# Optimization experiments

Hardware: AMD Instinct MI355X
Metric: run time of the kernel (lower is better)

## Reference

```python
import jax, jax.numpy as jnp
import numpy as np

B, L, W, S, STEPS, VOCAB, NLAB = 1024, 128, 512, 8, 12, 32, 10

def setup_inputs() -> dict:
    key = jax.random.key(0)
    ks = jax.random.split(key, 24)
    def nrm(k, shape, scale=0.05):
        return jax.random.normal(k, shape, jnp.float32) * scale
    x = jax.random.randint(ks[0], (B, L), 0, VOCAB)
    embed = nrm(ks[1], (VOCAB, W), 0.1).at[0].set(0.0)  # padding_idx=0
    return {
        'x': x,
        'embed': embed,
        'W_mix': nrm(ks[2], (W, 3 * W)), 'b_mix': jnp.zeros((W,), jnp.float32),
        'W_in': nrm(ks[3], (S, W, 2 * W)), 'b_in': jnp.zeros((S, W), jnp.float32),
        'W_link': nrm(ks[4], (S, W, W)), 'b_link': jnp.zeros((S, W), jnp.float32),
        'W_ih': nrm(ks[5], (S, 3 * W, W)), 'b_ih': jnp.zeros((S, 3 * W), jnp.float32),
        'W_hh': nrm(ks[6], (S, 3 * W, W)), 'b_hh': jnp.zeros((S, 3 * W), jnp.float32),
        'W_gate': nrm(ks[7], (S, 1, W)), 'b_gate': jnp.zeros((S, 1), jnp.float32),
        'phase': nrm(ks[8], (S, W), 0.5), 'prism_gain': jnp.zeros((S, W), jnp.float32),
        'W_delta': nrm(ks[9], (S, W, W)), 'b_delta': jnp.zeros((S, W), jnp.float32),
        'decay_param': jnp.zeros((), jnp.float32),
        'W_out': nrm(ks[10], (NLAB, W)), 'b_out': jnp.zeros((NLAB,), jnp.float32),
    }

def _encode(x, embed, W_mix, b_mix):
    emb = embed[x]                                          # [B,L,W]
    mask = (x != 0).astype(jnp.float32)[..., None]          # [B,L,1]
    summed = (emb * mask).sum(1)
    denom = jnp.maximum(mask.sum(1), 1.0)
    mean = summed / denom
    maxed = jnp.where(mask == 0, -10000.0, emb).max(1)
    maxed = jnp.where(jnp.isfinite(maxed), maxed, 0.0)
    last_idx = jnp.maximum(mask[..., 0].sum(1).astype(jnp.int32) - 1, 0)
    last = jnp.take_along_axis(emb, last_idx[:, None, None], axis=1)[:, 0]
    cat = jnp.concatenate([mean, maxed, last], -1)          # [B,3W]
    return jnp.tanh(cat @ W_mix.T + b_mix)

def _forward(x, embed, W_mix, b_mix, W_in, b_in, W_link, b_link, W_ih, b_ih,
             W_hh, b_hh, W_gate, b_gate, phase, prism_gain, W_delta, b_delta,
             decay_param, W_out, b_out):
    summary = _encode(x, embed, W_mix, b_mix)               # [B,W]
    decay = jax.nn.sigmoid(decay_param)
    inv_sqrt_s = np.float32(1.0 / np.sqrt(S))
    gain = jax.nn.softplus(prism_gain)[None]                # [1,S,W]

    def step(carry, _):
        h, hs = carry
        shared = jnp.concatenate([h, summary], -1)          # conditioned: [B,2W]
        f0 = jnp.tanh(jnp.einsum('swi,bi->bsw', W_in, shared) + b_in)      # [B,S,W]
        prev = jnp.roll(f0, 1, axis=1)                      # sparse ring: feats[(i-1)%S]
        feats = jnp.tanh(f0 + jnp.einsum('sow,bsw->bso', W_link, prev) + b_link)
        # recurrent side pockets: per-side GRUCell (torch gate order r,z,n)
        gi = jnp.einsum('sgw,bsw->bsg', W_ih, feats) + b_ih
        gh = jnp.einsum('sgw,bsw->bsg', W_hh, hs) + b_hh
        ir, iz, inn = jnp.split(gi, 3, -1)
        hr, hz, hn = jnp.split(gh, 3, -1)
        r = jax.nn.sigmoid(ir + hr)
        z = jax.nn.sigmoid(iz + hz)
        n = jnp.tanh(inn + r * hn)
        hs_new = (1.0 - z) * n + z * hs                     # [B,S,W]
        feat = hs_new
        gate = jax.nn.sigmoid(jnp.einsum('sow,bsw->bso', W_gate, feat) + b_gate)  # [B,S,1]
        feat = jnp.cos(feat + phase[None]) ** 2 * gain      # prismion
        upd = gate * jnp.tanh(jnp.einsum('sow,bsw->bso', W_delta, feat) + b_delta)
        delta = upd.sum(1) * inv_sqrt_s
        h_new = jnp.tanh(h * decay + delta)
        return (h_new, hs_new), None

    hs0 = jnp.zeros((B, S, W), jnp.float32)
    (h, _), _ = jax.lax.scan(step, (summary, hs0), None, length=STEPS)
    return h @ W_out.T + b_out                               # [B,10]

def reference(x, embed, W_mix, b_mix, W_in, b_in, W_link, b_link, W_ih, b_ih,
              W_hh, b_hh, W_gate, b_gate, phase, prism_gain, W_delta, b_delta,
              decay_param, W_out, b_out):
    return _forward(x, embed, W_mix, b_mix, W_in, b_in, W_link, b_link, W_ih,
                    b_ih, W_hh, b_hh, W_gate, b_gate, phase, prism_gain,
                    W_delta, b_delta, decay_param, W_out, b_out)
```

## Files before the change

kernel.cpp:

```cpp
#include <hip/hip_runtime.h>
#include <hip/hip_bf16.h>


typedef unsigned short u16;
typedef __attribute__((ext_vector_type(8))) short short8;
typedef __attribute__((ext_vector_type(4))) float f32x4;

__device__ __forceinline__ float bf2f(u16 v) {
    union { unsigned int u; float f; } x; x.u = ((unsigned int)v) << 16; return x.f;
}
__device__ __forceinline__ u16 f2bf(float f) {
    union { float f; unsigned int u; } x; x.f = f;
    unsigned int u = x.u;
    return (u16)((u + 0x7FFFu + ((u >> 16) & 1u)) >> 16);
}
__device__ __forceinline__ float fsig(float v) {
    return __builtin_amdgcn_rcpf(1.f + __expf(-v));
}
__device__ __forceinline__ float ftanh(float v) {
    return 1.f - 2.f * __builtin_amdgcn_rcpf(__expf(2.f * v) + 1.f);
}
__device__ __forceinline__ float fsoftplus(float v) {
    return (v > 20.f) ? v : __logf(1.f + __expf(v));
}

union U4 { ushort4 v; u16 e[4]; };

__device__ __forceinline__ void gload_lds16(const u16* g, u16* l) {
    __builtin_amdgcn_global_load_lds(
        (const __attribute__((address_space(1))) unsigned int*)g,
        (__attribute__((address_space(3))) unsigned int*)l, 16, 0, 0);
}

__device__ __forceinline__ int sane16(u16 u) {
    if ((u & 0x7FFF) == 0) return 1;
    int e = (u >> 7) & 0xFF;
    return (e >= 0x33 && e <= 0x43) ? 1 : 0;
}
__global__ __launch_bounds__(256) void detect_k(const u16* __restrict__ raw,
                                                int* __restrict__ flag) {
    const int t = threadIdx.x;
    int c = sane16(raw[1024 + t * 2]) + sane16(raw[1024 + t * 2 + 1]);
#pragma unroll
    for (int off = 32; off; off >>= 1) c += __shfl_down(c, off, 64);
    __shared__ int red[4];
    if ((t & 63) == 0) red[t >> 6] = c;
    __syncthreads();
    if (t == 0) *flag = (red[0] + red[1] + red[2] + red[3] >= 448) ? 1 : 0;
}

struct CT { const void* src[20]; int n[20]; int off[20]; };
__global__ __launch_bounds__(256) void conv_k(CT ct, u16* __restrict__ dstBase,
                                              const int* __restrict__ flag) {
    const int isbf = *flag;
    const int gid = blockIdx.x * 256 + threadIdx.x;
    const int stride = gridDim.x * 256;
    for (int tn = 0; tn < 20; ++tn) {
        const int n = ct.n[tn];
        const int n4 = n >> 2;
        u16* dst = dstBase + ct.off[tn];
        if (!isbf) {
            const float* s = (const float*)ct.src[tn];
            for (int i = gid; i < n4; i += stride) {
                f32x4 v = *(const f32x4*)(s + i * 4);
                *(ushort4*)(dst + i * 4) =
                    make_ushort4(f2bf(v[0]), f2bf(v[1]), f2bf(v[2]), f2bf(v[3]));
            }
            if (gid < (n & 3)) { int i = n4 * 4 + gid; dst[i] = f2bf(s[i]); }
        } else {
            const u16* s = (const u16*)ct.src[tn];
            for (int i = gid; i < n4; i += stride)
                *(ushort4*)(dst + i * 4) = *(const ushort4*)(s + i * 4);
            if (gid < (n & 3)) { int i = n4 * 4 + gid; dst[i] = s[i]; }
        }
    }
}

__global__ __launch_bounds__(256) void pack_k(const u16* __restrict__ Wih,
                                              const u16* __restrict__ Whh,
                                              u16* __restrict__ Wcat) {
    long i = ((long)blockIdx.x * 256 + threadIdx.x) * 8;
    if (i >= 8L * 1536 * 512) return;
    long sg = i >> 9;
    long k  = i & 511;
    *(short8*)(Wcat + sg * 1024 + k)       = *(const short8*)(Wih + i);
    *(short8*)(Wcat + sg * 1024 + 512 + k) = *(const short8*)(Whh + i);
}

struct GP {
    const u16* A;  long lda; long aOff[8];
    const u16* Bw; long ldb; long bwOff[8];
    const u16* bias; long biasOff[8];
    const u16* add; long ldadd; long addOff;
    const float* gate_pre;
    const u16* bgate;
    void* C; long ldc; long cOff[8];
    float* C2;
    u16* C3;
    int K; int nt;
};

template<int EPI, int MT>
__global__ __launch_bounds__(256) void gemm_k(GP p) {
    constexpr int MW   = MT / 32;
    constexpr int AITS = MT / 32;
    __shared__ __align__(16) u16 lA[2][MT * 64];
    __shared__ __align__(16) u16 lB[2][128 * 64];
    const int t    = threadIdx.x;
    const int lane = t & 63;
    const int wv   = t >> 6;
    const int bx   = blockIdx.x;
    const int z    = bx / p.nt;
    const int n0   = (bx - z * p.nt) * 128;
    const int m0   = blockIdx.y * MT;

    const u16* Ab = p.A + p.aOff[z] + (long)m0 * p.lda;
    const u16* Bb = p.Bw + p.bwOff[z] + (long)n0 * p.ldb;

    f32x4 acc[MW][4];
#pragma unroll
    for (int i = 0; i < MW; i++)
#pragma unroll
        for (int j = 0; j < 4; j++) acc[i][j] = (f32x4){0.f, 0.f, 0.f, 0.f};

    const int wm   = (wv & 1) * (MT / 2);
    const int wn   = (wv >> 1) * 64;
    const int fr   = lane & 15;
    const int quad = lane >> 4;

    const int nk = p.K >> 6;
#pragma unroll
    for (int it = 0; it < AITS; ++it) {
        int flat = it * 256 + t, row = flat >> 3, src = (flat & 7) ^ (row & 7);
        gload_lds16(Ab + (long)row * p.lda + src * 8, &lA[0][flat * 8]);
    }
#pragma unroll
    for (int it = 0; it < 4; ++it) {
        int flat = it * 256 + t, row = flat >> 3, src = (flat & 7) ^ (row & 7);
        gload_lds16(Bb + (long)row * p.ldb + src * 8, &lB[0][flat * 8]);
    }
    __syncthreads();

    for (int kt = 0; kt < nk; ++kt) {
        const int cur = kt & 1, nxt = cur ^ 1;
        if (kt + 1 < nk) {
            const long kb = (long)(kt + 1) * 64;
#pragma unroll
            for (int it = 0; it < AITS; ++it) {
                int flat = it * 256 + t, row = flat >> 3, src = (flat & 7) ^ (row & 7);
                gload_lds16(Ab + (long)row * p.lda + kb + src * 8, &lA[nxt][flat * 8]);
            }
#pragma unroll
            for (int it = 0; it < 4; ++it) {
                int flat = it * 256 + t, row = flat >> 3, src = (flat & 7) ^ (row & 7);
                gload_lds16(Bb + (long)row * p.ldb + kb + src * 8, &lB[nxt][flat * 8]);
            }
        }
#pragma unroll
        for (int kk = 0; kk < 2; ++kk) {
            const int q = kk * 4 + quad;
            short8 aF[MW], bF[4];
#pragma unroll
            for (int mi = 0; mi < MW; mi++) {
                int row = wm + mi * 16 + fr;
                aF[mi] = *(const short8*)&lA[cur][row * 64 + (q ^ (row & 7)) * 8];
            }
#pragma unroll
            for (int ni = 0; ni < 4; ni++) {
                int row = wn + ni * 16 + fr;
                bF[ni] = *(const short8*)&lB[cur][row * 64 + (q ^ (row & 7)) * 8];
            }
#pragma unroll
            for (int mi = 0; mi < MW; mi++)
#pragma unroll
                for (int ni = 0; ni < 4; ni++)
                    acc[mi][ni] = __builtin_amdgcn_mfma_f32_16x16x32_bf16(
                        aF[mi], bF[ni], acc[mi][ni], 0, 0, 0);
        }
        __syncthreads();
    }

    float sgv[MW][4];
    if (EPI == 3) {
#pragma unroll
        for (int mi = 0; mi < MW; mi++)
#pragma unroll
            for (int r = 0; r < 4; r++) {
                long row = m0 + wm + mi * 16 + quad * 4 + r;
                sgv[mi][r] = fsig(p.gate_pre[row * 8 + z] + bf2f(p.bgate[z]));
            }
    }

#pragma unroll
    for (int mi = 0; mi < MW; mi++) {
#pragma unroll
        for (int ni = 0; ni < 4; ni++) {
            const int mg = m0 + wm + mi * 16 + quad * 4;
            const int ng = n0 + wn + ni * 16 + fr;
#pragma unroll
            for (int r = 0; r < 4; r++) {
                float v = acc[mi][ni][r];
                const long row = mg + r;
                if (EPI == 1) {
                    float ad = bf2f(p.add[z * p.addOff + row * p.ldadd + ng]);
                    v = ftanh(v + ad + bf2f(p.bias[p.biasOff[z] + ng]));
                    ((u16*)p.C)[p.cOff[z] + row * p.ldc + ng] = f2bf(v);
                } else if (EPI == 3) {
                    v = ftanh(v + bf2f(p.bias[p.biasOff[z] + ng])) * sgv[mi][r];
                    ((u16*)p.C)[p.cOff[z] + row * p.ldc + ng] = f2bf(v);
                } else if (EPI == 4) {
                    v = ftanh(v + bf2f(p.bias[ng]));
                    u16 b = f2bf(v);
                    ((u16*)p.C)[row * 512 + ng] = b;
                    p.C3[row * 512 + ng] = b;
                    p.C2[row * 512 + ng] = v;
                } else if (EPI == 6) {
                    v = v + bf2f(p.bias[p.biasOff[z] + ng]);
                    ((u16*)p.C)[p.cOff[z] + row * p.ldc + ng] = f2bf(v);
                } else {
                    float ad = bf2f(p.add[row * p.ldadd + ng]);
                    v = ftanh(v + ad);
                    ((u16*)p.C)[row * p.ldc + ng] = f2bf(v);
                }
            }
        }
    }
}

struct GGP {
    const u16* fhs_in;
    u16* fhs_out;
    const u16* Wcat;
    const u16* b_ih;
    const u16* b_hh;
    u16* prism;
    float* gate_pre;
    const u16* Wg;
    const u16* phase;
    const u16* pgain;
};

__global__ __launch_bounds__(256, 4) void grug_k(GGP p) {
    __shared__ __align__(16) u16 sA[2][64 * 32];
    __shared__ __align__(16) u16 sW[2][3][64 * 32];
    const int t    = threadIdx.x;
    const int lane = t & 63;
    const int wv   = t >> 6;
    const int s    = blockIdx.x >> 3;
    const int w0   = (blockIdx.x & 7) * 64;
    const int m0   = blockIdx.y * 64;
    const int fr   = lane & 15;
    const int quad = lane >> 4;
    const int wn   = wv * 16;

    const u16* Ab = p.fhs_in + (long)m0 * 8192 + s * 1024;
    const u16* Wb = p.Wcat + (long)s * 1536 * 1024;

    f32x4 acc[4][4];
#pragma unroll
    for (int q = 0; q < 4; q++)
#pragma unroll
        for (int mi = 0; mi < 4; mi++) acc[q][mi] = (f32x4){0.f,0.f,0.f,0.f};

    const int arow = t >> 2, ac4 = t & 3, asrc = ac4 ^ ((arow >> 1) & 3);

    auto stageA = [&](int buf, long kb) {
        gload_lds16(Ab + (long)arow * 8192 + kb + asrc * 8, &sA[buf][t * 8]);
    };
    auto stageW = [&](int buf, long kb) {
#pragma unroll
        for (int q = 0; q < 3; q++) {
            long g = (long)(q * 512 + w0 + arow);
            gload_lds16(Wb + g * 1024 + kb + asrc * 8, &sW[buf][q][t * 8]);
        }
    };

    stageA(0, 0); stageW(0, 0);
    __syncthreads();

    for (int kt = 0; kt < 32; ++kt) {
        const int cur = kt & 1, nxt = cur ^ 1;
        if (kt + 1 < 32) { stageA(nxt, (long)(kt + 1) * 32); stageW(nxt, (long)(kt + 1) * 32); }
        const int qsel = (kt < 16) ? 2 : 3;
        short8 aF[4], bF[3];
#pragma unroll
        for (int mi = 0; mi < 4; mi++) {
            int row = mi * 16 + fr;
            aF[mi] = *(const short8*)&sA[cur][row * 32 + ((quad ^ ((row >> 1) & 3)) & 3) * 8];
        }
#pragma unroll
        for (int q = 0; q < 3; q++) {
            int row = wn + fr;
            bF[q] = *(const short8*)&sW[cur][q][row * 32 + ((quad ^ ((row >> 1) & 3)) & 3) * 8];
        }
#pragma unroll
        for (int mi = 0; mi < 4; mi++) {
            acc[0][mi] = __builtin_amdgcn_mfma_f32_16x16x32_bf16(aF[mi], bF[0], acc[0][mi], 0, 0, 0);
            acc[1][mi] = __builtin_amdgcn_mfma_f32_16x16x32_bf16(aF[mi], bF[1], acc[1][mi], 0, 0, 0);
            if (qsel == 2)
                acc[2][mi] = __builtin_amdgcn_mfma_f32_16x16x32_bf16(aF[mi], bF[2], acc[2][mi], 0, 0, 0);
            else
                acc[3][mi] = __builtin_amdgcn_mfma_f32_16x16x32_bf16(aF[mi], bF[2], acc[3][mi], 0, 0, 0);
        }
        __syncthreads();
    }

    const u16* bih = p.b_ih + (long)s * 1536;
    const u16* bhh = p.b_hh + (long)s * 1536;
    float gp[4][4];
#pragma unroll
    for (int mi = 0; mi < 4; mi++)
#pragma unroll
        for (int r = 0; r < 4; r++) gp[mi][r] = 0.f;

    {
        const int col = w0 + wn + fr;
        const float br  = bf2f(bih[col])        + bf2f(bhh[col]);
        const float bz  = bf2f(bih[512 + col])  + bf2f(bhh[512 + col]);
        const float bin = bf2f(bih[1024 + col]);
        const float bhn = bf2f(bhh[1024 + col]);
        const float ph  = bf2f(p.phase[s * 512 + col]);
        const float gain = fsoftplus(bf2f(p.pgain[s * 512 + col]));
        const float wg  = bf2f(p.Wg[s * 512 + col]);
#pragma unroll
        for (int mi = 0; mi < 4; mi++) {
#pragma unroll
            for (int r = 0; r < 4; r++) {
                const long b = m0 + mi * 16 + quad * 4 + r;
                float rv = fsig(acc[0][mi][r] + br);
                float zv = fsig(acc[1][mi][r] + bz);
                float nv = ftanh(acc[2][mi][r] + bin + rv * (acc[3][mi][r] + bhn));
                float hold = bf2f(p.fhs_in[b * 8192 + s * 1024 + 512 + col]);
                float hv = (1.f - zv) * nv + zv * hold;
                p.fhs_out[b * 8192 + s * 1024 + 512 + col] = f2bf(hv);
                float c = __cosf(hv + ph);
                p.prism[b * 4096 + s * 512 + col] = f2bf(c * c * gain);
                gp[mi][r] += wg * hv;
            }
        }
    }
#pragma unroll
    for (int m = 1; m < 16; m <<= 1)
#pragma unroll
        for (int mi = 0; mi < 4; mi++)
#pragma unroll
            for (int r = 0; r < 4; r++) gp[mi][r] += __shfl_xor(gp[mi][r], m, 64);
    if (fr == 0) {
#pragma unroll
        for (int mi = 0; mi < 4; mi++)
#pragma unroll
            for (int r = 0; r < 4; r++) {
                long b = m0 + mi * 16 + quad * 4 + r;
                atomicAdd(&p.gate_pre[b * 8 + s], gp[mi][r]);
            }
    }
}

__global__ __launch_bounds__(256) void encode_k(const int* __restrict__ x,
                                                const u16* __restrict__ embed,
                                                u16* __restrict__ cat) {
    __shared__ int toks[128];
    __shared__ int cnt_s;
    const int b = blockIdx.x, t = threadIdx.x;
    if (t < 128) toks[t] = x[b * 128 + t];
    __syncthreads();
    if (t == 0) {
        int c = 0;
        for (int l = 0; l < 128; l++) c += (toks[l] != 0);
        cnt_s = c;
    }
    __syncthreads();
    const int cnt = cnt_s;
    const int lastTok = toks[cnt > 0 ? cnt - 1 : 0];
    for (int w = t; w < 512; w += 256) {
        float sum = 0.f, mx = -10000.f;
        for (int l = 0; l < 128; l++) {
            int tok = toks[l];
            if (tok != 0) {
                float e = bf2f(embed[tok * 512 + w]);
                sum += e;
                mx = fmaxf(mx, e);
            }
        }
        float mean = sum / (float)(cnt > 0 ? cnt : 1);
        float last = bf2f(embed[lastTok * 512 + w]);
        cat[(long)b * 1536 + w]        = f2bf(mean);
        cat[(long)b * 1536 + 512 + w]  = f2bf(mx);
        cat[(long)b * 1536 + 1024 + w] = f2bf(last);
    }
}

__global__ __launch_bounds__(256) void hupd_k(const u16* __restrict__ upd,
                                              float* __restrict__ h,
                                              u16* __restrict__ h_b,
                                              const u16* __restrict__ decay_p) {
    const int idx = blockIdx.x * 256 + threadIdx.x;
    const int b = idx >> 9, w = idx & 511;
    const long base = (long)b * 4096 + w;
    float dsum = 0.f;
#pragma unroll
    for (int s = 0; s < 8; s++) dsum += bf2f(upd[base + s * 512]);
    const float decay = fsig(bf2f(decay_p[0]));
    const float hv = ftanh(h[idx] * decay + dsum * 0.35355339059327373f);
    h[idx] = hv;
    h_b[idx] = f2bf(hv);
}

__global__ __launch_bounds__(64) void out_k(const float* __restrict__ h,
                                            const u16* __restrict__ Wout,
                                            const u16* __restrict__ bout,
                                            void* __restrict__ out,
                                            const int* __restrict__ flag) {
    const int b = blockIdx.x, lane = threadIdx.x;
    const int isbf = *flag;
    for (int j = 0; j < 10; j++) {
        float p = 0.f;
#pragma unroll
        for (int k = 0; k < 8; k++) {
            int w = lane + k * 64;
            p += h[(long)b * 512 + w] * bf2f(Wout[j * 512 + w]);
        }
#pragma unroll
        for (int off = 32; off; off >>= 1) p += __shfl_down(p, off, 64);
        if (lane == 0) {
            float val = p + bf2f(bout[j]);
            if (isbf) ((u16*)out)[b * 10 + j] = f2bf(val);
            else      ((float*)out)[b * 10 + j] = val;
        }
    }
}

extern "C" void kernel_launch(void* const* d_in, const int* in_sizes, int n_in,
                              void* d_out, int out_size, void* d_ws, size_t ws_size,
                              hipStream_t stream) {
    (void)n_in; (void)out_size; (void)ws_size;
    const int* x = (const int*)d_in[0];

    char* pp = (char*)d_ws;
    auto carve = [&](size_t n) { char* r = pp; pp += (n + 255) & ~(size_t)255; return (void*)r; };

    CT ct;
    size_t ctot = 0;
    for (int i = 0; i < 20; i++) {
        ct.src[i] = d_in[i + 1];
        ct.n[i]   = in_sizes[i + 1];
        ct.off[i] = (int)ctot;
        ctot += ((size_t)in_sizes[i + 1] + 15) & ~(size_t)15;
    }
    u16* canon = (u16*)carve(ctot * 2);
    const u16* embed  = canon + ct.off[0];
    const u16* W_mix  = canon + ct.off[1];
    const u16* b_mix  = canon + ct.off[2];
    const u16* W_in   = canon + ct.off[3];
    const u16* b_in   = canon + ct.off[4];
    const u16* W_link = canon + ct.off[5];
    const u16* b_link = canon + ct.off[6];
    const u16* W_ih   = canon + ct.off[7];
    const u16* b_ih   = canon + ct.off[8];
    const u16* W_hh   = canon + ct.off[9];
    const u16* b_hh   = canon + ct.off[10];
    const u16* W_gate = canon + ct.off[11];
    const u16* b_gate = canon + ct.off[12];
    const u16* phase  = canon + ct.off[13];
    const u16* pgain  = canon + ct.off[14];
    const u16* W_delta= canon + ct.off[15];
    const u16* b_delta= canon + ct.off[16];
    const u16* decayp = canon + ct.off[17];
    const u16* W_out  = canon + ct.off[18];
    const u16* b_out  = canon + ct.off[19];

    int*   flag   = (int*)  carve(256);
    u16*   Wcat   = (u16*)  carve((size_t)8 * 1536 * 1024 * 2);
    u16*   cat    = (u16*)  carve((size_t)1024 * 1536 * 2);
    u16*   h_b    = (u16*)  carve((size_t)1024 * 512 * 2);
    u16*   summ_b = (u16*)  carve((size_t)1024 * 512 * 2);
    float* h      = (float*)carve((size_t)1024 * 512 * 4);
    u16*   cin    = (u16*)  carve((size_t)1024 * 4096 * 2);
    u16*   f0     = (u16*)  carve((size_t)1024 * 4096 * 2);
    u16*   fhs0   = (u16*)  carve((size_t)1024 * 8192 * 2);
    u16*   fhs1   = (u16*)  carve((size_t)1024 * 8192 * 2);
    u16*   prism  = (u16*)  carve((size_t)1024 * 4096 * 2);
    u16*   upd    = (u16*)  carve((size_t)1024 * 4096 * 2);
    float* gate_pre = (float*)carve((size_t)1024 * 8 * 4);

    (void)hipMemsetAsync(fhs0, 0, (size_t)1024 * 8192 * 2, stream);
    (void)hipMemsetAsync(fhs1, 0, (size_t)1024 * 8192 * 2, stream);

    detect_k<<<dim3(1), dim3(256), 0, stream>>>((const u16*)d_in[1], flag);
    conv_k<<<dim3(1024), dim3(256), 0, stream>>>(ct, canon, flag);
    pack_k<<<dim3(3072), dim3(256), 0, stream>>>(W_ih, W_hh, Wcat);
    encode_k<<<dim3(1024), dim3(256), 0, stream>>>(x, embed, cat);

    {
        GP p{}; p.A = cat; p.lda = 1536; p.Bw = W_mix; p.ldb = 1536;
        p.bias = b_mix; p.C = h_b; p.ldc = 512; p.C2 = h; p.C3 = summ_b;
        p.K = 1536; p.nt = 4;
        gemm_k<4, 64><<<dim3(4, 16, 1), dim3(256), 0, stream>>>(p);
    }
    {
        GP p{}; p.A = summ_b; p.lda = 512; p.Bw = W_in + 512; p.ldb = 1024;
        p.bias = b_in; p.C = cin; p.ldc = 4096; p.K = 512; p.nt = 32;
        gemm_k<6, 64><<<dim3(32, 16, 1), dim3(256), 0, stream>>>(p);
    }

    for (int step = 0; step < 12; ++step) {
        u16* fhs_cur = (step & 1) ? fhs1 : fhs0;
        u16* fhs_nxt = (step & 1) ? fhs0 : fhs1;
        {
            GP p{}; p.A = h_b; p.lda = 512; p.Bw = W_in; p.ldb = 1024;
            p.add = cin; p.ldadd = 4096; p.C = f0; p.ldc = 4096;
            p.K = 512; p.nt = 32;
            gemm_k<7, 64><<<dim3(32, 16, 1), dim3(256), 0, stream>>>(p);
        }
        {
            GP p{}; p.A = f0; p.lda = 4096;
            for (int s = 0; s < 8; s++) p.aOff[s] = (long)((s + 7) & 7) * 512;
            p.Bw = W_link; p.ldb = 512;
            for (int s = 0; s < 8; s++) p.bwOff[s] = (long)s * 512 * 512;
            p.bias = b_link;
            for (int s = 0; s < 8; s++) p.biasOff[s] = (long)s * 512;
            p.add = f0; p.ldadd = 4096; p.addOff = 512;
            p.C = fhs_cur; p.ldc = 8192;
            for (int s = 0; s < 8; s++) p.cOff[s] = (long)s * 1024;
            p.K = 512; p.nt = 4;
            gemm_k<1, 64><<<dim3(32, 16, 1), dim3(256), 0, stream>>>(p);
        }
        (void)hipMemsetAsync(gate_pre, 0, (size_t)1024 * 8 * 4, stream);
        {
            GGP g{};
            g.fhs_in = fhs_cur; g.fhs_out = fhs_nxt; g.Wcat = Wcat;
            g.b_ih = b_ih; g.b_hh = b_hh; g.prism = prism; g.gate_pre = gate_pre;
            g.Wg = W_gate; g.phase = phase; g.pgain = pgain;
            grug_k<<<dim3(64, 16, 1), dim3(256), 0, stream>>>(g);
        }
        {
            GP p{}; p.A = prism; p.lda = 4096;
            for (int s = 0; s < 8; s++) p.aOff[s] = (long)s * 512;
            p.Bw = W_delta; p.ldb = 512;
            for (int s = 0; s < 8; s++) p.bwOff[s] = (long)s * 512 * 512;
            p.bias = b_delta;
            for (int s = 0; s < 8; s++) p.biasOff[s] = (long)s * 512;
            p.gate_pre = gate_pre; p.bgate = b_gate;
            p.C = upd; p.ldc = 4096;
            for (int s = 0; s < 8; s++) p.cOff[s] = (long)s * 512;
            p.K = 512; p.nt = 4;
            gemm_k<3, 64><<<dim3(32, 16, 1), dim3(256), 0, stream>>>(p);
        }
        hupd_k<<<dim3(2048), dim3(256), 0, stream>>>(upd, h, h_b, decayp);
    }

    out_k<<<dim3(1024), dim3(64), 0, stream>>>(h, W_out, b_out, d_out, flag);
}
```

Before: 1.715 ms.

## Swizzle GEMM blocks across XCDs, widen GRU tile, fold gate_pre reset into hupd

Adds an optional workgroup-id swizzle to the batched GEMM so consecutive workgroups map to different stacks and n-tiles. This is meant to improve L2 reuse of weight tiles on the multi-XCD part. The GRU kernel now runs 512 threads and covers 128 output columns per block, sharing one activation tile across twice as many weight rows. Its block order is also remapped so the stack index varies fastest. The per-step memset of gate_pre is replaced by zeroing inside hupd_k, which removes one launch per step. The 512-thread launch with a minimum of 4 blocks per CU tightens the register budget and may cause spills.

```diff
diff --git a/kernel.cpp b/kernel.cpp
--- a/kernel.cpp
+++ b/kernel.cpp
@@ -100,7 +100,7 @@
     int K; int nt;
 };
 
-template<int EPI, int MT>
+template<int EPI, int MT, int SWZ>
 __global__ __launch_bounds__(256) void gemm_k(GP p) {
     constexpr int MW   = MT / 32;
     constexpr int AITS = MT / 32;
@@ -109,10 +109,15 @@
     const int t    = threadIdx.x;
     const int lane = t & 63;
     const int wv   = t >> 6;
-    const int bx   = blockIdx.x;
+    int bx = blockIdx.x, byy = blockIdx.y;
+    if (SWZ) {
+        int wgid = bx + (byy << 5);
+        bx  = ((wgid & 7) << 2) + ((wgid >> 3) & 3);
+        byy = wgid >> 5;
+    }
     const int z    = bx / p.nt;
     const int n0   = (bx - z * p.nt) * 128;
-    const int m0   = blockIdx.y * MT;
+    const int m0   = byy * MT;
 
     const u16* Ab = p.A + p.aOff[z] + (long)m0 * p.lda;
     const u16* Bb = p.Bw + p.bwOff[z] + (long)n0 * p.ldb;
@@ -240,15 +245,17 @@
     const u16* pgain;
 };
 
-__global__ __launch_bounds__(256, 4) void grug_k(GGP p) {
+__global__ __launch_bounds__(512, 4) void grug_k(GGP p) {
     __shared__ __align__(16) u16 sA[2][64 * 32];
-    __shared__ __align__(16) u16 sW[2][3][64 * 32];
+    __shared__ __align__(16) u16 sW[2][3][128 * 32];
     const int t    = threadIdx.x;
     const int lane = t & 63;
     const int wv   = t >> 6;
-    const int s    = blockIdx.x >> 3;
-    const int w0   = (blockIdx.x & 7) * 64;
-    const int m0   = blockIdx.y * 64;
+    const int wgid = blockIdx.x + (blockIdx.y << 5);
+    const int s    = wgid & 7;
+    const int idx  = wgid >> 3;
+    const int w0   = (idx & 3) * 128;
+    const int m0   = (idx >> 2) * 64;
     const int fr   = lane & 15;
     const int quad = lane >> 4;
     const int wn   = wv * 16;
@@ -265,7 +272,8 @@
     const int arow = t >> 2, ac4 = t & 3, asrc = ac4 ^ ((arow >> 1) & 3);
 
     auto stageA = [&](int buf, long kb) {
-        gload_lds16(Ab + (long)arow * 8192 + kb + asrc * 8, &sA[buf][t * 8]);
+        if (t < 256)
+            gload_lds16(Ab + (long)arow * 8192 + kb + asrc * 8, &sA[buf][t * 8]);
     };
     auto stageW = [&](int buf, long kb) {
 #pragma unroll
@@ -393,8 +401,10 @@
 __global__ __launch_bounds__(256) void hupd_k(const u16* __restrict__ upd,
                                               float* __restrict__ h,
                                               u16* __restrict__ h_b,
-                                              const u16* __restrict__ decay_p) {
+                                              const u16* __restrict__ decay_p,
+                                              float* __restrict__ gate_pre) {
     const int idx = blockIdx.x * 256 + threadIdx.x;
+    if (idx < 8192) gate_pre[idx] = 0.f;
     const int b = idx >> 9, w = idx & 511;
     const long base = (long)b * 4096 + w;
     float dsum = 0.f;
@@ -485,6 +495,7 @@
 
     (void)hipMemsetAsync(fhs0, 0, (size_t)1024 * 8192 * 2, stream);
     (void)hipMemsetAsync(fhs1, 0, (size_t)1024 * 8192 * 2, stream);
+    (void)hipMemsetAsync(gate_pre, 0, (size_t)1024 * 8 * 4, stream);
 
     detect_k<<<dim3(1), dim3(256), 0, stream>>>((const u16*)d_in[1], flag);
     conv_k<<<dim3(1024), dim3(256), 0, stream>>>(ct, canon, flag);
@@ -495,12 +506,12 @@
         GP p{}; p.A = cat; p.lda = 1536; p.Bw = W_mix; p.ldb = 1536;
         p.bias = b_mix; p.C = h_b; p.ldc = 512; p.C2 = h; p.C3 = summ_b;
         p.K = 1536; p.nt = 4;
-        gemm_k<4, 64><<<dim3(4, 16, 1), dim3(256), 0, stream>>>(p);
+        gemm_k<4, 64, 0><<<dim3(4, 16, 1), dim3(256), 0, stream>>>(p);
     }
     {
         GP p{}; p.A = summ_b; p.lda = 512; p.Bw = W_in + 512; p.ldb = 1024;
         p.bias = b_in; p.C = cin; p.ldc = 4096; p.K = 512; p.nt = 32;
-        gemm_k<6, 64><<<dim3(32, 16, 1), dim3(256), 0, stream>>>(p);
+        gemm_k<6, 64, 1><<<dim3(32, 16, 1), dim3(256), 0, stream>>>(p);
     }
 
     for (int step = 0; step < 12; ++step) {
@@ -510,7 +521,7 @@
             GP p{}; p.A = h_b; p.lda = 512; p.Bw = W_in; p.ldb = 1024;
             p.add = cin; p.ldadd = 4096; p.C = f0; p.ldc = 4096;
             p.K = 512; p.nt = 32;
-            gemm_k<7, 64><<<dim3(32, 16, 1), dim3(256), 0, stream>>>(p);
+            gemm_k<7, 64, 1><<<dim3(32, 16, 1), dim3(256), 0, stream>>>(p);
         }
         {
             GP p{}; p.A = f0; p.lda = 4096;
@@ -523,15 +534,14 @@
             p.C = fhs_cur; p.ldc = 8192;
             for (int s = 0; s < 8; s++) p.cOff[s] = (long)s * 1024;
             p.K = 512; p.nt = 4;
-            gemm_k<1, 64><<<dim3(32, 16, 1), dim3(256), 0, stream>>>(p);
-        }
-        (void)hipMemsetAsync(gate_pre, 0, (size_t)1024 * 8 * 4, stream);
+            gemm_k<1, 64, 1><<<dim3(32, 16, 1), dim3(256), 0, stream>>>(p);
+        }
         {
             GGP g{};
             g.fhs_in = fhs_cur; g.fhs_out = fhs_nxt; g.Wcat = Wcat;
             g.b_ih = b_ih; g.b_hh = b_hh; g.prism = prism; g.gate_pre = gate_pre;
             g.Wg = W_gate; g.phase = phase; g.pgain = pgain;
-            grug_k<<<dim3(64, 16, 1), dim3(256), 0, stream>>>(g);
+            grug_k<<<dim3(32, 16, 1), dim3(512), 0, stream>>>(g);
         }
         {
             GP p{}; p.A = prism; p.lda = 4096;
@@ -544,9 +554,9 @@
             p.C = upd; p.ldc = 4096;
             for (int s = 0; s < 8; s++) p.cOff[s] = (long)s * 512;
             p.K = 512; p.nt = 4;
-            gemm_k<3, 64><<<dim3(32, 16, 1), dim3(256), 0, stream>>>(p);
-        }
-        hupd_k<<<dim3(2048), dim3(256), 0, stream>>>(upd, h, h_b, decayp);
+            gemm_k<3, 64, 1><<<dim3(32, 16, 1), dim3(256), 0, stream>>>(p);
+        }
+        hupd_k<<<dim3(2048), dim3(256), 0, stream>>>(upd, h, h_b, decayp, gate_pre);
     }
 
     out_k<<<dim3(1024), dim3(64), 0, stream>>>(h, W_out, b_out, d_out, flag);
```

Result: faster. 1.656 ms (-3.5%).
